# Kernel tuning notes

Measured on AMD Instinct MI355X. Metric: run time of the kernel, lower is better.

The kernel has to match this reference:

```python
import jax, jax.numpy as jnp
import numpy as np

N_HEADS = 4
N_GROUPS = 32
EPS = 1e-5


def setup_inputs() -> dict:
    key = jax.random.key(0)
    ks = jax.random.split(key, 6)
    c = 512
    x = jax.random.normal(ks[0], (4, c, 64, 64), dtype=jnp.float32)
    # conv1x1 weights ~ kaiming-ish scale
    s = 1.0 / np.sqrt(c)
    wq = jax.random.normal(ks[1], (c, c), dtype=jnp.float32) * s
    wk = jax.random.normal(ks[2], (c, c), dtype=jnp.float32) * s
    wv = jax.random.normal(ks[3], (c, c), dtype=jnp.float32) * s
    wp = jax.random.normal(ks[4], (c, c), dtype=jnp.float32) * s
    zeros = jnp.zeros((c,), dtype=jnp.float32)
    return {
        "x": x,
        "gn_w": jnp.ones((c,), dtype=jnp.float32), "gn_b": zeros,
        "wq": wq, "bq": zeros, "wk": wk, "bk": zeros,
        "wv": wv, "bv": zeros, "wp": wp, "bp": zeros,
    }


def _group_norm(x, w, b):
    bsz, c, h, wd = x.shape
    xg = x.reshape(bsz, N_GROUPS, c // N_GROUPS, h, wd)
    mean = xg.mean(axis=(2, 3, 4), keepdims=True)
    var = xg.var(axis=(2, 3, 4), keepdims=True)
    xg = (xg - mean) * jax.lax.rsqrt(var + EPS)
    x = xg.reshape(bsz, c, h, wd)
    return x * w[None, :, None, None] + b[None, :, None, None]


def _conv1x1(x, w, b):
    # x: (b,c,h,w), w: (out,in) -> (b,out,h,w)
    return jnp.einsum('bchw,oc->bohw', x, w) + b[None, :, None, None]


def reference(x, gn_w, gn_b, wq, bq, wk, bk, wv, bv, wp, bp):
    bsz, c, h, wd = x.shape
    hd = c // N_HEADS
    hw = h * wd
    x_n = _group_norm(x, gn_w, gn_b)
    q = _conv1x1(x_n, wq, bq)
    k = _conv1x1(x_n, wk, bk)
    v = _conv1x1(x_n, wv, bv)

    def to_heads(t):
        # (b,c,h,w) -> (b, n_heads, hw, head_dim)
        return t.reshape(bsz, N_HEADS, hd, hw).transpose(0, 1, 3, 2)

    q, k, v = to_heads(q), to_heads(k), to_heads(v)
    scale = hd ** (-0.5)
    attn = jnp.einsum('bhqd,bhkd->bhqk', q, k) * scale  # (b,H,hw,hw)
    attn = jax.nn.softmax(attn, axis=-1)
    out = jnp.einsum('bhqk,bhkd->bhqd', attn, v)
    out = out.transpose(0, 1, 3, 2).reshape(bsz, c, h, wd)
    out = _conv1x1(out, wp, bp)
    return x + out
```

## Files before the change

kernel.cpp:

```cpp
#include <hip/hip_runtime.h>
#include <math.h>

typedef __attribute__((ext_vector_type(8))) short short8;
typedef __attribute__((ext_vector_type(4))) float floatx4;
typedef __attribute__((ext_vector_type(16))) float floatx16;
typedef __attribute__((ext_vector_type(8))) unsigned short ushort8v;
typedef __attribute__((ext_vector_type(4))) unsigned short ushort4v;

#define HW 4096
#define CCH 512
#define NB 4
#define NH 4
#define HD 128

__device__ __forceinline__ unsigned short f2bf(float f) {
    union { float f; unsigned int u; } c; c.f = f;
    unsigned int u = c.u;
    u += 0x7FFFu + ((u >> 16) & 1u);
    return (unsigned short)(u >> 16);
}

__global__ void conv_w(const float* __restrict__ w0, const float* __restrict__ w1,
                       const float* __restrict__ w2, const float* __restrict__ w3,
                       unsigned short* __restrict__ dst) {
    const float* src = blockIdx.y == 0 ? w0 : blockIdx.y == 1 ? w1 : blockIdx.y == 2 ? w2 : w3;
    unsigned short* d = dst + (size_t)blockIdx.y * 262144;
    int i = blockIdx.x * 256 + threadIdx.x;
    float4 v = ((const float4*)src)[i];
    ushort4v o;
    o[0] = f2bf(v.x); o[1] = f2bf(v.y); o[2] = f2bf(v.z); o[3] = f2bf(v.w);
    ((ushort4v*)d)[i] = o;
}

__global__ void gn_stats(const float* __restrict__ x, float* __restrict__ stats) {
    int bg = blockIdx.x;
    int b = bg >> 5, g = bg & 31;
    const float4* p = (const float4*)(x + ((size_t)b * CCH + g * 16) * HW);
    float s = 0.f, ss = 0.f;
    for (int i = threadIdx.x; i < 16384; i += 256) {
        float4 v = p[i];
        s  += v.x + v.y + v.z + v.w;
        ss += v.x * v.x + v.y * v.y + v.z * v.z + v.w * v.w;
    }
    #pragma unroll
    for (int off = 32; off > 0; off >>= 1) {
        s  += __shfl_down(s, off, 64);
        ss += __shfl_down(ss, off, 64);
    }
    __shared__ float sm[4], sm2[4];
    int wid = threadIdx.x >> 6;
    if ((threadIdx.x & 63) == 0) { sm[wid] = s; sm2[wid] = ss; }
    __syncthreads();
    if (threadIdx.x == 0) {
        float ts = sm[0] + sm[1] + sm[2] + sm[3];
        float tss = sm2[0] + sm2[1] + sm2[2] + sm2[3];
        float mean = ts * (1.f / 65536.f);
        float var = tss * (1.f / 65536.f) - mean * mean;
        stats[bg * 2] = mean;
        stats[bg * 2 + 1] = rsqrtf(var + 1e-5f);
    }
}

__global__ void gn_apply(const float* __restrict__ x, const float* __restrict__ gnw,
                         const float* __restrict__ gnb, const float* __restrict__ stats,
                         unsigned short* __restrict__ xt) {
    int s = blockIdx.x * 256 + threadIdx.x;
    int g = blockIdx.y, b = blockIdx.z;
    float mean = stats[(b * 32 + g) * 2];
    float rstd = stats[(b * 32 + g) * 2 + 1];
    const float* xb = x + ((size_t)b * CCH + g * 16) * HW + s;
    unsigned short outv[16];
    #pragma unroll
    for (int cl = 0; cl < 16; cl++) {
        int c = g * 16 + cl;
        float v = xb[(size_t)cl * HW];
        v = (v - mean) * rstd * gnw[c] + gnb[c];
        outv[cl] = f2bf(v);
    }
    unsigned short* dst = xt + ((size_t)b * HW + s) * CCH + g * 16;
    *(ushort8v*)dst       = *(ushort8v*)&outv[0];
    *(ushort8v*)(dst + 8) = *(ushort8v*)&outv[8];
}

#define LDP 72
template <int MODE>
__global__ __launch_bounds__(256, 2) void gemm_nt(
    const unsigned short* __restrict__ A, long long aStride,
    const unsigned short* __restrict__ Bm, long long bStride,
    const float* __restrict__ bias, float scale,
    const float* __restrict__ resid, long long rStride,
    void* __restrict__ Cp, long long cStride, int ldc) {
    __shared__ unsigned short lA[128 * LDP];
    __shared__ unsigned short lB[128 * LDP];
    const int tid = threadIdx.x;
    const int lane = tid & 63;
    const int wid = tid >> 6;
    const int z = blockIdx.z;
    const unsigned short* Ab = A + (size_t)z * aStride + (size_t)blockIdx.x * 128 * 512;
    const unsigned short* Bb = Bm + (size_t)z * bStride + (size_t)blockIdx.y * 128 * 512;

    floatx4 acc[4][4];
    #pragma unroll
    for (int i = 0; i < 4; i++)
        #pragma unroll
        for (int j = 0; j < 4; j++) acc[i][j] = (floatx4)0.f;

    const int wm = (wid >> 1) * 64;
    const int wn = (wid & 1) * 64;
    const int l15 = lane & 15;
    const int l4 = lane >> 4;

    for (int k0 = 0; k0 < 512; k0 += 64) {
        #pragma unroll
        for (int i = 0; i < 4; i++) {
            int idx = i * 256 + tid;
            int row = idx >> 3;
            int kc = (idx & 7) * 8;
            *(ushort8v*)&lA[row * LDP + kc] = *(const ushort8v*)&Ab[(size_t)row * 512 + k0 + kc];
            *(ushort8v*)&lB[row * LDP + kc] = *(const ushort8v*)&Bb[(size_t)row * 512 + k0 + kc];
        }
        __syncthreads();
        #pragma unroll
        for (int kk = 0; kk < 2; kk++) {
            short8 af[4], bf[4];
            #pragma unroll
            for (int i = 0; i < 4; i++)
                af[i] = *(const short8*)&lA[(wm + i * 16 + l15) * LDP + kk * 32 + l4 * 8];
            #pragma unroll
            for (int j = 0; j < 4; j++)
                bf[j] = *(const short8*)&lB[(wn + j * 16 + l15) * LDP + kk * 32 + l4 * 8];
            #pragma unroll
            for (int i = 0; i < 4; i++)
                #pragma unroll
                for (int j = 0; j < 4; j++)
                    acc[i][j] = __builtin_amdgcn_mfma_f32_16x16x32_bf16(af[i], bf[j], acc[i][j], 0, 0, 0);
        }
        __syncthreads();
    }

    long long m0 = (long long)blockIdx.x * 128 + wm;
    long long n0 = (long long)blockIdx.y * 128 + wn;
    if (MODE == 0) {
        unsigned short* C = (unsigned short*)Cp + (size_t)z * cStride;
        #pragma unroll
        for (int i = 0; i < 4; i++)
            #pragma unroll
            for (int j = 0; j < 4; j++) {
                long long col = n0 + j * 16 + l15;
                float bv = bias[col];
                #pragma unroll
                for (int r = 0; r < 4; r++) {
                    long long row = m0 + i * 16 + l4 * 4 + r;
                    C[row * ldc + col] = f2bf((acc[i][j][r] + bv) * scale);
                }
            }
    } else if (MODE == 1) {
        float* C = (float*)Cp + (size_t)z * cStride;
        const float* R = resid + (size_t)z * rStride;
        #pragma unroll
        for (int i = 0; i < 4; i++)
            #pragma unroll
            for (int j = 0; j < 4; j++)
                #pragma unroll
                for (int r = 0; r < 4; r++) {
                    long long row = m0 + i * 16 + l4 * 4 + r;
                    long long col = n0 + j * 16 + l15;
                    C[row * ldc + col] = acc[i][j][r] + bias[row] + R[row * ldc + col];
                }
    } else {
        unsigned short* C = (unsigned short*)Cp + (size_t)z * cStride;
        #pragma unroll
        for (int i = 0; i < 4; i++)
            #pragma unroll
            for (int j = 0; j < 4; j++)
                #pragma unroll
                for (int r = 0; r < 4; r++) {
                    long long row = m0 + i * 16 + l4 * 4 + r;
                    long long col = n0 + j * 16 + l15;
                    C[row * ldc + col] = f2bf(acc[i][j][r] + bias[row]);
                }
    }
}

#define LQP 136
#define LTP 72
__global__ __launch_bounds__(256, 2) void attn_kern(
    const unsigned short* __restrict__ Qb, const unsigned short* __restrict__ Kb,
    const unsigned short* __restrict__ Vt, unsigned short* __restrict__ Ob) {
    __shared__ unsigned short lk[2][64 * LQP];
    __shared__ unsigned short lvt[2][128 * LTP];
    const int tid = threadIdx.x;
    const int lane = tid & 63;
    const int w = tid >> 6;
    const int l31 = lane & 31;
    const int l1 = lane >> 5;
    const int q0 = blockIdx.x * 128;
    const int h = blockIdx.y, b = blockIdx.z;
    const size_t headOff = (size_t)h * HD;
    const size_t batchRow = (size_t)b * HW;
    const unsigned short* VtB = Vt + ((size_t)b * CCH + headOff) * HW;

    short8 qf[8];
    #pragma unroll
    for (int kd = 0; kd < 8; kd++)
        qf[kd] = *(const short8*)&Qb[(batchRow + q0 + w * 32 + l31) * 512
                                     + headOff + kd * 16 + l1 * 8];

    short8 onesf;
    #pragma unroll
    for (int e = 0; e < 8; e++) onesf[e] = (short)0x3F80;

    floatx16 acc_o[4];
    floatx16 acc_l;
    acc_l = (floatx16)0.f;
    #pragma unroll
    for (int dj = 0; dj < 4; dj++) acc_o[dj] = (floatx16)0.f;

    ushort8v kreg[4], vreg[4];
    #pragma unroll
    for (int i = 0; i < 4; i++) {
        int idx = i * 256 + tid;
        kreg[i] = *(const ushort8v*)&Kb[(batchRow + (idx >> 4)) * 512 + headOff + (idx & 15) * 8];
        vreg[i] = *(const ushort8v*)&VtB[(size_t)(idx >> 3) * HW + (idx & 7) * 8];
    }
    #pragma unroll
    for (int i = 0; i < 4; i++) {
        int idx = i * 256 + tid;
        *(ushort8v*)&lk[0][(idx >> 4) * LQP + (idx & 15) * 8] = kreg[i];
        *(ushort8v*)&lvt[0][(idx >> 3) * LTP + (idx & 7) * 8] = vreg[i];
    }
    __syncthreads();

    int cur = 0;
    for (int kt = 0; kt < 64; kt++) {
        const unsigned short* lkc  = lk[cur];
        const unsigned short* lvtc = lvt[cur];

        if (kt < 63) {
            int t0n = (kt + 1) * 64;
            #pragma unroll
            for (int i = 0; i < 4; i++) {
                int idx = i * 256 + tid;
                kreg[i] = *(const ushort8v*)&Kb[(batchRow + t0n + (idx >> 4)) * 512 + headOff + (idx & 15) * 8];
                vreg[i] = *(const ushort8v*)&VtB[(size_t)(idx >> 3) * HW + t0n + (idx & 7) * 8];
            }
        }

        floatx16 sa[2];
        sa[0] = (floatx16)0.f;
        sa[1] = (floatx16)0.f;
        __builtin_amdgcn_s_setprio(1);
        #pragma unroll
        for (int kd = 0; kd < 8; kd++) {
            short8 kf0 = *(const short8*)&lkc[(l31) * LQP + kd * 16 + l1 * 8];
            short8 kf1 = *(const short8*)&lkc[(32 + l31) * LQP + kd * 16 + l1 * 8];
            sa[0] = __builtin_amdgcn_mfma_f32_32x32x16_bf16(kf0, qf[kd], sa[0], 0, 0, 0);
            sa[1] = __builtin_amdgcn_mfma_f32_32x32x16_bf16(kf1, qf[kd], sa[1], 0, 0, 0);
        }
        __builtin_amdgcn_s_setprio(0);

        #pragma unroll
        for (int tb = 0; tb < 2; tb++)
            #pragma unroll
            for (int r = 0; r < 16; r++)
                sa[tb][r] = __builtin_amdgcn_exp2f(sa[tb][r]);

        short8 paf[4];
        #pragma unroll
        for (int tb = 0; tb < 2; tb++) {
            unsigned int wv[4][2];
            #pragma unroll
            for (int g = 0; g < 4; g++) {
                asm("v_cvt_pk_bf16_f32 %0, %1, %2" : "=v"(wv[g][0])
                    : "v"(sa[tb][4 * g + 0]), "v"(sa[tb][4 * g + 1]));
                asm("v_cvt_pk_bf16_f32 %0, %1, %2" : "=v"(wv[g][1])
                    : "v"(sa[tb][4 * g + 2]), "v"(sa[tb][4 * g + 3]));
            }
            #pragma unroll
            for (int hh = 0; hh < 2; hh++) {
                unsigned int a0 = wv[2 * hh][0], b0 = wv[2 * hh + 1][0];
                unsigned int a1 = wv[2 * hh][1], b1 = wv[2 * hh + 1][1];
                asm("v_permlane32_swap_b32 %0, %1" : "+v"(a0), "+v"(b0));
                asm("v_permlane32_swap_b32 %0, %1" : "+v"(a1), "+v"(b1));
                union { unsigned int u[4]; short8 s8; } f;
                f.u[0] = a0; f.u[1] = a1; f.u[2] = b0; f.u[3] = b1;
                paf[2 * tb + hh] = f.s8;
            }
        }

        __builtin_amdgcn_s_setprio(1);
        #pragma unroll
        for (int tw = 0; tw < 4; tw++) {
            acc_l = __builtin_amdgcn_mfma_f32_32x32x16_bf16(paf[tw], onesf, acc_l, 0, 0, 0);
            #pragma unroll
            for (int dj = 0; dj < 4; dj++) {
                short8 vv = *(const short8*)&lvtc[(dj * 32 + l31) * LTP + tw * 16 + l1 * 8];
                acc_o[dj] = __builtin_amdgcn_mfma_f32_32x32x16_bf16(paf[tw], vv, acc_o[dj], 0, 0, 0);
            }
        }
        __builtin_amdgcn_s_setprio(0);

        if (kt < 63) {
            int nxt = cur ^ 1;
            #pragma unroll
            for (int i = 0; i < 4; i++) {
                int idx = i * 256 + tid;
                *(ushort8v*)&lk[nxt][(idx >> 4) * LQP + (idx & 15) * 8] = kreg[i];
                *(ushort8v*)&lvt[nxt][(idx >> 3) * LTP + (idx & 7) * 8] = vreg[i];
            }
            __syncthreads();
            cur = nxt;
        }
    }

    #pragma unroll
    for (int g = 0; g < 4; g++)
        #pragma unroll
        for (int p = 0; p < 4; p++) {
            int reg = 4 * g + p;
            float rl = 1.f / acc_l[reg];
            int qr = p + 8 * g + 4 * l1;
            size_t row = batchRow + q0 + w * 32 + qr;
            #pragma unroll
            for (int dj = 0; dj < 4; dj++)
                Ob[row * 512 + headOff + dj * 32 + l31] = f2bf(acc_o[dj][reg] * rl);
        }
}

extern "C" void kernel_launch(void* const* d_in, const int* in_sizes, int n_in,
                              void* d_out, int out_size, void* d_ws, size_t ws_size,
                              hipStream_t stream) {
    const float* x   = (const float*)d_in[0];
    const float* gnw = (const float*)d_in[1];
    const float* gnb = (const float*)d_in[2];
    const float* wq  = (const float*)d_in[3];
    const float* bq  = (const float*)d_in[4];
    const float* wk  = (const float*)d_in[5];
    const float* bk  = (const float*)d_in[6];
    const float* wv  = (const float*)d_in[7];
    const float* bv  = (const float*)d_in[8];
    const float* wp  = (const float*)d_in[9];
    const float* bp  = (const float*)d_in[10];
    float* out = (float*)d_out;

    const size_t NE = (size_t)NB * HW * CCH;
    unsigned short* ws16 = (unsigned short*)d_ws;
    unsigned short* XT = ws16;
    unsigned short* Qb = ws16 + NE;
    unsigned short* Kb = ws16 + 2 * NE;
    unsigned short* Vt = ws16 + 3 * NE;
    unsigned short* Wb = ws16 + 4 * NE;
    float* stats = (float*)(ws16 + 4 * NE + 4 * 262144);

    const float qscale = 0.08838834764831845f * 1.4426950408889634f;

    conv_w<<<dim3(256, 4), 256, 0, stream>>>(wq, wk, wv, wp, Wb);
    gn_stats<<<128, 256, 0, stream>>>(x, stats);
    gn_apply<<<dim3(16, 32, 4), 256, 0, stream>>>(x, gnw, gnb, stats, XT);

    gemm_nt<0><<<dim3(128, 4, 1), 256, 0, stream>>>(XT, 0, Wb + 0 * 262144, 0, bq, qscale, nullptr, 0, Qb, 0, 512);
    gemm_nt<0><<<dim3(128, 4, 1), 256, 0, stream>>>(XT, 0, Wb + 1 * 262144, 0, bk, 1.f, nullptr, 0, Kb, 0, 512);
    gemm_nt<2><<<dim3(4, 32, 4), 256, 0, stream>>>(Wb + 2 * 262144, 0, XT, (long long)HW * 512, bv, 1.f,
                                                   nullptr, 0, Vt, (long long)CCH * HW, HW);

    unsigned short* Ob = XT;
    attn_kern<<<dim3(32, NH, NB), 256, 0, stream>>>(Qb, Kb, Vt, Ob);

    gemm_nt<1><<<dim3(4, 32, 4), 256, 0, stream>>>(Wb + 3 * 262144, 0, Ob, (long long)HW * 512, bp, 1.f,
                                                   x, (long long)CCH * HW, out, (long long)CCH * HW, HW);
}
```

Before: 355.9 us.

## Double-buffer GEMM LDS tiles, merge Q/K projections, interleave softmax with PV

The projection GEMM now uses two LDS buffers and register prefetch, so global loads for the next K-tile overlap the MFMAs on the current one and one barrier per iteration is dropped. The Q and K projections run as a single launch over a z=2 grid, with the K bias passed through the resid pointer. In attention, exp/pack of the second score block is placed after the PV MFMAs of the first block so ALU and matrix work can overlap. Doubling LDS per block may reduce occupancy under the launch bound of 2 blocks.

```diff
diff --git a/kernel.cpp b/kernel.cpp
--- a/kernel.cpp
+++ b/kernel.cpp
@@ -90,8 +90,8 @@
     const float* __restrict__ bias, float scale,
     const float* __restrict__ resid, long long rStride,
     void* __restrict__ Cp, long long cStride, int ldc) {
-    __shared__ unsigned short lA[128 * LDP];
-    __shared__ unsigned short lB[128 * LDP];
+    __shared__ unsigned short lA[2][128 * LDP];
+    __shared__ unsigned short lB[2][128 * LDP];
     const int tid = threadIdx.x;
     const int lane = tid & 63;
     const int wid = tid >> 6;
@@ -109,49 +109,80 @@
     const int wn = (wid & 1) * 64;
     const int l15 = lane & 15;
     const int l4 = lane >> 4;
-
-    for (int k0 = 0; k0 < 512; k0 += 64) {
-        #pragma unroll
-        for (int i = 0; i < 4; i++) {
-            int idx = i * 256 + tid;
-            int row = idx >> 3;
-            int kc = (idx & 7) * 8;
-            *(ushort8v*)&lA[row * LDP + kc] = *(const ushort8v*)&Ab[(size_t)row * 512 + k0 + kc];
-            *(ushort8v*)&lB[row * LDP + kc] = *(const ushort8v*)&Bb[(size_t)row * 512 + k0 + kc];
-        }
-        __syncthreads();
+    const int srow = tid >> 3;
+    const int skc  = (tid & 7) * 8;
+
+    ushort8v ar[4], br[4];
+    #pragma unroll
+    for (int i = 0; i < 4; i++) {
+        int row = srow + i * 32;
+        ar[i] = *(const ushort8v*)&Ab[(size_t)row * 512 + skc];
+        br[i] = *(const ushort8v*)&Bb[(size_t)row * 512 + skc];
+    }
+    #pragma unroll
+    for (int i = 0; i < 4; i++) {
+        int row = srow + i * 32;
+        *(ushort8v*)&lA[0][row * LDP + skc] = ar[i];
+        *(ushort8v*)&lB[0][row * LDP + skc] = br[i];
+    }
+    __syncthreads();
+
+    int cur = 0;
+    #pragma unroll 1
+    for (int t = 0; t < 8; t++) {
+        if (t < 7) {
+            int k0 = (t + 1) * 64;
+            #pragma unroll
+            for (int i = 0; i < 4; i++) {
+                int row = srow + i * 32;
+                ar[i] = *(const ushort8v*)&Ab[(size_t)row * 512 + k0 + skc];
+                br[i] = *(const ushort8v*)&Bb[(size_t)row * 512 + k0 + skc];
+            }
+        }
         #pragma unroll
         for (int kk = 0; kk < 2; kk++) {
             short8 af[4], bf[4];
             #pragma unroll
             for (int i = 0; i < 4; i++)
-                af[i] = *(const short8*)&lA[(wm + i * 16 + l15) * LDP + kk * 32 + l4 * 8];
+                af[i] = *(const short8*)&lA[cur][(wm + i * 16 + l15) * LDP + kk * 32 + l4 * 8];
             #pragma unroll
             for (int j = 0; j < 4; j++)
-                bf[j] = *(const short8*)&lB[(wn + j * 16 + l15) * LDP + kk * 32 + l4 * 8];
+                bf[j] = *(const short8*)&lB[cur][(wn + j * 16 + l15) * LDP + kk * 32 + l4 * 8];
             #pragma unroll
             for (int i = 0; i < 4; i++)
                 #pragma unroll
                 for (int j = 0; j < 4; j++)
                     acc[i][j] = __builtin_amdgcn_mfma_f32_16x16x32_bf16(af[i], bf[j], acc[i][j], 0, 0, 0);
         }
-        __syncthreads();
+        if (t < 7) {
+            int nxt = cur ^ 1;
+            #pragma unroll
+            for (int i = 0; i < 4; i++) {
+                int row = srow + i * 32;
+                *(ushort8v*)&lA[nxt][row * LDP + skc] = ar[i];
+                *(ushort8v*)&lB[nxt][row * LDP + skc] = br[i];
+            }
+            __syncthreads();
+            cur = nxt;
+        }
     }
 
     long long m0 = (long long)blockIdx.x * 128 + wm;
     long long n0 = (long long)blockIdx.y * 128 + wn;
-    if (MODE == 0) {
+    if (MODE == 0 || MODE == 3) {
         unsigned short* C = (unsigned short*)Cp + (size_t)z * cStride;
+        const float* bptr = (MODE == 3 && z == 1) ? resid : bias;
+        float sc = (MODE == 3 && z == 1) ? 1.f : scale;
         #pragma unroll
         for (int i = 0; i < 4; i++)
             #pragma unroll
             for (int j = 0; j < 4; j++) {
                 long long col = n0 + j * 16 + l15;
-                float bv = bias[col];
+                float bv = bptr[col];
                 #pragma unroll
                 for (int r = 0; r < 4; r++) {
                     long long row = m0 + i * 16 + l4 * 4 + r;
-                    C[row * ldc + col] = f2bf((acc[i][j][r] + bv) * scale);
+                    C[row * ldc + col] = f2bf((acc[i][j][r] + bv) * sc);
                 }
             }
     } else if (MODE == 1) {
@@ -246,57 +277,97 @@
             }
         }
 
-        floatx16 sa[2];
-        sa[0] = (floatx16)0.f;
-        sa[1] = (floatx16)0.f;
+        floatx16 sa0 = (floatx16)0.f;
+        floatx16 sa1 = (floatx16)0.f;
         __builtin_amdgcn_s_setprio(1);
         #pragma unroll
         for (int kd = 0; kd < 8; kd++) {
             short8 kf0 = *(const short8*)&lkc[(l31) * LQP + kd * 16 + l1 * 8];
             short8 kf1 = *(const short8*)&lkc[(32 + l31) * LQP + kd * 16 + l1 * 8];
-            sa[0] = __builtin_amdgcn_mfma_f32_32x32x16_bf16(kf0, qf[kd], sa[0], 0, 0, 0);
-            sa[1] = __builtin_amdgcn_mfma_f32_32x32x16_bf16(kf1, qf[kd], sa[1], 0, 0, 0);
+            sa0 = __builtin_amdgcn_mfma_f32_32x32x16_bf16(kf0, qf[kd], sa0, 0, 0, 0);
+            sa1 = __builtin_amdgcn_mfma_f32_32x32x16_bf16(kf1, qf[kd], sa1, 0, 0, 0);
         }
         __builtin_amdgcn_s_setprio(0);
 
-        #pragma unroll
-        for (int tb = 0; tb < 2; tb++)
-            #pragma unroll
-            for (int r = 0; r < 16; r++)
-                sa[tb][r] = __builtin_amdgcn_exp2f(sa[tb][r]);
-
-        short8 paf[4];
-        #pragma unroll
-        for (int tb = 0; tb < 2; tb++) {
+        short8 paf0, paf1;
+        {
+            #pragma unroll
+            for (int r = 0; r < 16; r++) sa0[r] = __builtin_amdgcn_exp2f(sa0[r]);
             unsigned int wv[4][2];
             #pragma unroll
             for (int g = 0; g < 4; g++) {
                 asm("v_cvt_pk_bf16_f32 %0, %1, %2" : "=v"(wv[g][0])
-                    : "v"(sa[tb][4 * g + 0]), "v"(sa[tb][4 * g + 1]));
+                    : "v"(sa0[4 * g + 0]), "v"(sa0[4 * g + 1]));
                 asm("v_cvt_pk_bf16_f32 %0, %1, %2" : "=v"(wv[g][1])
-                    : "v"(sa[tb][4 * g + 2]), "v"(sa[tb][4 * g + 3]));
-            }
-            #pragma unroll
-            for (int hh = 0; hh < 2; hh++) {
-                unsigned int a0 = wv[2 * hh][0], b0 = wv[2 * hh + 1][0];
-                unsigned int a1 = wv[2 * hh][1], b1 = wv[2 * hh + 1][1];
-                asm("v_permlane32_swap_b32 %0, %1" : "+v"(a0), "+v"(b0));
-                asm("v_permlane32_swap_b32 %0, %1" : "+v"(a1), "+v"(b1));
-                union { unsigned int u[4]; short8 s8; } f;
-                f.u[0] = a0; f.u[1] = a1; f.u[2] = b0; f.u[3] = b1;
-                paf[2 * tb + hh] = f.s8;
-            }
+                    : "v"(sa0[4 * g + 2]), "v"(sa0[4 * g + 3]));
+            }
+            unsigned int a0 = wv[0][0], b0 = wv[1][0], a1 = wv[0][1], b1 = wv[1][1];
+            asm("v_permlane32_swap_b32 %0, %1" : "+v"(a0), "+v"(b0));
+            asm("v_permlane32_swap_b32 %0, %1" : "+v"(a1), "+v"(b1));
+            union { unsigned int u[4]; short8 s8; } f0;
+            f0.u[0] = a0; f0.u[1] = a1; f0.u[2] = b0; f0.u[3] = b1;
+            paf0 = f0.s8;
+            unsigned int c0 = wv[2][0], d0 = wv[3][0], c1 = wv[2][1], d1 = wv[3][1];
+            asm("v_permlane32_swap_b32 %0, %1" : "+v"(c0), "+v"(d0));
+            asm("v_permlane32_swap_b32 %0, %1" : "+v"(c1), "+v"(d1));
+            union { unsigned int u[4]; short8 s8; } f1;
+            f1.u[0] = c0; f1.u[1] = c1; f1.u[2] = d0; f1.u[3] = d1;
+            paf1 = f1.s8;
         }
 
         __builtin_amdgcn_s_setprio(1);
-        #pragma unroll
-        for (int tw = 0; tw < 4; tw++) {
-            acc_l = __builtin_amdgcn_mfma_f32_32x32x16_bf16(paf[tw], onesf, acc_l, 0, 0, 0);
-            #pragma unroll
-            for (int dj = 0; dj < 4; dj++) {
-                short8 vv = *(const short8*)&lvtc[(dj * 32 + l31) * LTP + tw * 16 + l1 * 8];
-                acc_o[dj] = __builtin_amdgcn_mfma_f32_32x32x16_bf16(paf[tw], vv, acc_o[dj], 0, 0, 0);
-            }
+        acc_l = __builtin_amdgcn_mfma_f32_32x32x16_bf16(paf0, onesf, acc_l, 0, 0, 0);
+        #pragma unroll
+        for (int dj = 0; dj < 4; dj++) {
+            short8 vv = *(const short8*)&lvtc[(dj * 32 + l31) * LTP + 0 * 16 + l1 * 8];
+            acc_o[dj] = __builtin_amdgcn_mfma_f32_32x32x16_bf16(paf0, vv, acc_o[dj], 0, 0, 0);
+        }
+        acc_l = __builtin_amdgcn_mfma_f32_32x32x16_bf16(paf1, onesf, acc_l, 0, 0, 0);
+        #pragma unroll
+        for (int dj = 0; dj < 4; dj++) {
+            short8 vv = *(const short8*)&lvtc[(dj * 32 + l31) * LTP + 1 * 16 + l1 * 8];
+            acc_o[dj] = __builtin_amdgcn_mfma_f32_32x32x16_bf16(paf1, vv, acc_o[dj], 0, 0, 0);
+        }
+        __builtin_amdgcn_s_setprio(0);
+
+        short8 paf2, paf3;
+        {
+            #pragma unroll
+            for (int r = 0; r < 16; r++) sa1[r] = __builtin_amdgcn_exp2f(sa1[r]);
+            unsigned int wv[4][2];
+            #pragma unroll
+            for (int g = 0; g < 4; g++) {
+                asm("v_cvt_pk_bf16_f32 %0, %1, %2" : "=v"(wv[g][0])
+                    : "v"(sa1[4 * g + 0]), "v"(sa1[4 * g + 1]));
+                asm("v_cvt_pk_bf16_f32 %0, %1, %2" : "=v"(wv[g][1])
+                    : "v"(sa1[4 * g + 2]), "v"(sa1[4 * g + 3]));
+            }
+            unsigned int a0 = wv[0][0], b0 = wv[1][0], a1 = wv[0][1], b1 = wv[1][1];
+            asm("v_permlane32_swap_b32 %0, %1" : "+v"(a0), "+v"(b0));
+            asm("v_permlane32_swap_b32 %0, %1" : "+v"(a1), "+v"(b1));
+            union { unsigned int u[4]; short8 s8; } f2;
+            f2.u[0] = a0; f2.u[1] = a1; f2.u[2] = b0; f2.u[3] = b1;
+            paf2 = f2.s8;
+            unsigned int c0 = wv[2][0], d0 = wv[3][0], c1 = wv[2][1], d1 = wv[3][1];
+            asm("v_permlane32_swap_b32 %0, %1" : "+v"(c0), "+v"(d0));
+            asm("v_permlane32_swap_b32 %0, %1" : "+v"(c1), "+v"(d1));
+            union { unsigned int u[4]; short8 s8; } f3;
+            f3.u[0] = c0; f3.u[1] = c1; f3.u[2] = d0; f3.u[3] = d1;
+            paf3 = f3.s8;
+        }
+
+        __builtin_amdgcn_s_setprio(1);
+        acc_l = __builtin_amdgcn_mfma_f32_32x32x16_bf16(paf2, onesf, acc_l, 0, 0, 0);
+        #pragma unroll
+        for (int dj = 0; dj < 4; dj++) {
+            short8 vv = *(const short8*)&lvtc[(dj * 32 + l31) * LTP + 2 * 16 + l1 * 8];
+            acc_o[dj] = __builtin_amdgcn_mfma_f32_32x32x16_bf16(paf2, vv, acc_o[dj], 0, 0, 0);
+        }
+        acc_l = __builtin_amdgcn_mfma_f32_32x32x16_bf16(paf3, onesf, acc_l, 0, 0, 0);
+        #pragma unroll
+        for (int dj = 0; dj < 4; dj++) {
+            short8 vv = *(const short8*)&lvtc[(dj * 32 + l31) * LTP + 3 * 16 + l1 * 8];
+            acc_o[dj] = __builtin_amdgcn_mfma_f32_32x32x16_bf16(paf3, vv, acc_o[dj], 0, 0, 0);
         }
         __builtin_amdgcn_s_setprio(0);
 
@@ -358,8 +429,8 @@
     gn_stats<<<128, 256, 0, stream>>>(x, stats);
     gn_apply<<<dim3(16, 32, 4), 256, 0, stream>>>(x, gnw, gnb, stats, XT);
 
-    gemm_nt<0><<<dim3(128, 4, 1), 256, 0, stream>>>(XT, 0, Wb + 0 * 262144, 0, bq, qscale, nullptr, 0, Qb, 0, 512);
-    gemm_nt<0><<<dim3(128, 4, 1), 256, 0, stream>>>(XT, 0, Wb + 1 * 262144, 0, bk, 1.f, nullptr, 0, Kb, 0, 512);
+    gemm_nt<3><<<dim3(128, 4, 2), 256, 0, stream>>>(XT, 0, Wb, 262144, bq, qscale, bk, 0,
+                                                    Qb, (long long)NE, 512);
     gemm_nt<2><<<dim3(4, 32, 4), 256, 0, stream>>>(Wb + 2 * 262144, 0, XT, (long long)HW * 512, bv, 1.f,
                                                    nullptr, 0, Vt, (long long)CCH * HW, HW);
 
```

Result: faster. 346.8 us (-2.6%).
